# Kernel optimization log

Hardware: AMD Instinct MI355X
Metric: run time of the kernel (lower is better)

The kernel has to match this reference:

```python
import jax, jax.numpy as jnp
import numpy as np

NUM_HEADS = 16


def setup_inputs() -> dict:
    key = jax.random.key(0)
    ks = jax.random.split(key, 7)
    E = 1024
    s = 0.02
    return {
        "x": jax.random.normal(ks[0], (2, 2048, E), dtype=jnp.float32),
        "Wq": jax.random.normal(ks[1], (E, E), dtype=jnp.float32) * s,
        "bq": jax.random.normal(ks[2], (E,), dtype=jnp.float32) * s,
        "Wk": jax.random.normal(ks[3], (E, E), dtype=jnp.float32) * s,
        "bk": jax.random.normal(ks[4], (E,), dtype=jnp.float32) * s,
        "Wv": jax.random.normal(ks[5], (E, E), dtype=jnp.float32) * s,
        "bv": jax.random.normal(ks[6], (E,), dtype=jnp.float32) * s,
    }


def reference(x, Wq, bq, Wk, bk, Wv, bv):
    b, s, e = x.shape
    h = NUM_HEADS
    d = e // h  # head_dim = 64
    # nn.Linear: y = x @ W^T + b
    q = x @ Wq.T + bq
    k = x @ Wk.T + bk
    v = x @ Wv.T + bv
    # Faithful reshape chain from the source: (b,s,e)->(b,s,h,d)->(-1,s,d)
    # (raw reshape, NO transpose, matching the original buggy layout)
    q = q.reshape(b, s, h, d).reshape(-1, s, d)
    k = k.reshape(b, s, h, d).reshape(-1, s, d)
    v = v.reshape(b, s, h, d).reshape(-1, s, d)
    # Scaled scores; note the source returns qk @ v (softmax result discarded)
    scale = 1.0 / np.sqrt(d).astype(np.float32)
    qk = jnp.einsum('bqd,bkd->bqk', q, k) * scale  # [b*h, s, s]
    out = jnp.einsum('bqk,bkd->bqd', qk, v)        # [b*h, s, d]
    return out
```

## Files before the change

### kernel.cpp

```cpp
#include <hip/hip_runtime.h>
#include <hip/hip_bf16.h>


#define E_DIM 1024
#define N_ROWS 4096

typedef __attribute__((ext_vector_type(8))) short bf16x8;
typedef __attribute__((ext_vector_type(4))) float f32x4;

#define QB_U 0
#define XB_U 12582912
#define WB_U 16777216
#define P_F  9961472

__device__ __forceinline__ unsigned short f2b(float f) {
    union { float f; unsigned int i; } c; c.f = f;
    unsigned int r = c.i + 0x7FFFu + ((c.i >> 16) & 1u);
    return (unsigned short)(r >> 16);
}

__device__ __forceinline__ uint4 pack8(const f32x4 a, const f32x4 b) {
    uint4 o;
    o.x = (unsigned)f2b(a[0]) | ((unsigned)f2b(a[1]) << 16);
    o.y = (unsigned)f2b(a[2]) | ((unsigned)f2b(a[3]) << 16);
    o.z = (unsigned)f2b(b[0]) | ((unsigned)f2b(b[1]) << 16);
    o.w = (unsigned)f2b(b[2]) | ((unsigned)f2b(b[3]) << 16);
    return o;
}

__device__ __forceinline__ uint2 packfrag(const f32x4 a, float b) {
    uint2 v;
    v.x = (unsigned)f2b(a[0] + b) | ((unsigned)f2b(a[1] + b) << 16);
    v.y = (unsigned)f2b(a[2] + b) | ((unsigned)f2b(a[3] + b) << 16);
    return v;
}

typedef __attribute__((address_space(1))) const void* gptr_t;
typedef __attribute__((address_space(3))) void* lptr_t;
__device__ __forceinline__ void gl_lds16(const void* g, void* l) {
    __builtin_amdgcn_global_load_lds((gptr_t)g, (lptr_t)l, 16, 0, 0);
}

__device__ __forceinline__ int sw_idx(int row, int r) {
    return row * 64 + (((((r) >> 3) & 7) ^ (row & 7)) << 3) + (r & 7);
}

__device__ __forceinline__ int sw128(int row, int r) {
    return row * 128 + ((((r >> 3) ^ (row & 7)) & 15) << 3) + (r & 7);
}

__global__ __launch_bounds__(256) void cvt_bf16(
    const float* __restrict__ x,  const float* __restrict__ wq,
    const float* __restrict__ wk, const float* __restrict__ wv,
    unsigned short* __restrict__ dst0)
{
    const int seg = blockIdx.y;
    const float* __restrict__ src;
    unsigned short* __restrict__ dst;
    if (seg < 4) { src = x + (size_t)seg * 1048576; dst = dst0 + (size_t)seg * 1048576; }
    else {
        src = (seg == 4) ? wq : (seg == 5) ? wk : wv;
        dst = dst0 + 4194304 + (size_t)(seg - 4) * 1048576;
    }
    const int i = blockIdx.x * 256 + threadIdx.x;
    const float4 a = *(const float4*)(src + (size_t)i * 8);
    const float4 b = *(const float4*)(src + (size_t)i * 8 + 4);
    uint4 o;
    o.x = (unsigned)f2b(a.x) | ((unsigned)f2b(a.y) << 16);
    o.y = (unsigned)f2b(a.z) | ((unsigned)f2b(a.w) << 16);
    o.z = (unsigned)f2b(b.x) | ((unsigned)f2b(b.y) << 16);
    o.w = (unsigned)f2b(b.z) | ((unsigned)f2b(b.w) << 16);
    *(uint4*)(dst + (size_t)i * 8) = o;
}

__device__ __forceinline__ void gemm_loop(
    const unsigned short* __restrict__ Xb, const unsigned short* __restrict__ W,
    unsigned short* Als, unsigned short* Bls,
    int m0, int n0, int w, int lane, f32x4 (&acc)[4][4])
{
    const int quad = lane >> 4;
    const int fm   = lane & 15;
    const int sw8  = fm & 7;
    const int srow = lane >> 3;
    const int skc  = ((lane & 7) ^ (lane >> 3)) * 8;
    const int wm = (w >> 1) * 64;
    const int wn = (w & 1) * 64;

    for (int k0 = 0; k0 < E_DIM; k0 += 64) {
        #pragma unroll
        for (int c = 0; c < 4; ++c) {
            const int r = w * 32 + c * 8;
            gl_lds16((const void*)(Xb + (size_t)(m0 + r + srow) * E_DIM + k0 + skc),
                     (void*)((char*)Als + r * 128 + lane * 16));
            gl_lds16((const void*)(W + (size_t)(n0 + r + srow) * E_DIM + k0 + skc),
                     (void*)((char*)Bls + r * 128 + lane * 16));
        }
        __syncthreads();

        #pragma unroll
        for (int kk = 0; kk < 2; ++kk) {
            const int slot = ((kk * 4 + quad) ^ sw8) * 8;
            bf16x8 af[4], bf[4];
            #pragma unroll
            for (int t = 0; t < 4; ++t) {
                af[t] = *(const bf16x8*)(Als + (wm + t * 16 + fm) * 64 + slot);
                bf[t] = *(const bf16x8*)(Bls + (wn + t * 16 + fm) * 64 + slot);
            }
            #pragma unroll
            for (int rt = 0; rt < 4; ++rt)
                #pragma unroll
                for (int ct = 0; ct < 4; ++ct)
                    acc[rt][ct] = __builtin_amdgcn_mfma_f32_16x16x32_bf16(
                        af[rt], bf[ct], acc[rt][ct], 0, 0, 0);
        }
        __syncthreads();
    }
}

__global__ __launch_bounds__(256, 3) void qkvkt768(
    const unsigned short* __restrict__ Xb,
    const unsigned short* __restrict__ Wb,
    const float* __restrict__ bq, const float* __restrict__ bk,
    const float* __restrict__ bv,
    unsigned short* __restrict__ qkv,
    float* __restrict__ P)
{
    __shared__ __align__(16) unsigned short S[16384];

    const int b    = blockIdx.x;
    const int tid  = threadIdx.x;
    const int w    = tid >> 6;
    const int lane = tid & 63;
    const int quad = lane >> 4;
    const int fm   = lane & 15;
    const int sw8  = fm & 7;
    const int rbase = quad * 4;
    const int srow = lane >> 3;
    const int skc  = ((lane & 7) ^ (lane >> 3)) * 8;

    if (b >= 512) {
        const int idx = b - 512;
        const int m0 = (idx & 31) * 128;
        const int n0 = (idx >> 5) * 128;
        const int wm = (w >> 1) * 64;
        const int wn = (w & 1) * 64;

        f32x4 acc[4][4];
        #pragma unroll
        for (int i = 0; i < 4; ++i)
            #pragma unroll
            for (int j = 0; j < 4; ++j)
                acc[i][j] = f32x4{0.f, 0.f, 0.f, 0.f};

        gemm_loop(Xb, Wb, S, S + 8192, m0, n0, w, lane, acc);

        float bcol[4];
        #pragma unroll
        for (int ct = 0; ct < 4; ++ct) bcol[ct] = bq[n0 + wn + ct * 16 + fm];

        #pragma unroll
        for (int rt = 0; rt < 4; ++rt) {
            #pragma unroll
            for (int ct = 0; ct < 4; ++ct) {
                #pragma unroll
                for (int r = 0; r < 4; ++r) {
                    const int row = m0 + wm + rt * 16 + rbase + r;
                    const int col = n0 + wn + ct * 16 + fm;
                    qkv[(size_t)row * E_DIM + col] = f2b(acc[rt][ct][r] + bcol[ct]);
                }
            }
        }
        return;
    }

    const int bx = b >> 4;
    const int hy = b & 15;
    const int m0 = bx * 128;
    const int n0 = hy * 64;
    const unsigned short* __restrict__ WK = Wb + 1048576;
    const unsigned short* __restrict__ WV = Wb + 2097152;

    unsigned short* Xls = S;
    unsigned short* Kls = S + 8192;
    unsigned short* Vls = S + 12288;

    const int wm = w * 32;

    f32x4 acck[2][4], accv[2][4];
    #pragma unroll
    for (int t = 0; t < 2; ++t)
        #pragma unroll
        for (int n = 0; n < 4; ++n) {
            acck[t][n] = f32x4{0.f, 0.f, 0.f, 0.f};
            accv[t][n] = f32x4{0.f, 0.f, 0.f, 0.f};
        }

    for (int k0 = 0; k0 < E_DIM; k0 += 64) {
        #pragma unroll
        for (int c = 0; c < 4; ++c) {
            const int r = w * 32 + c * 8;
            gl_lds16((const void*)(Xb + (size_t)(m0 + r + srow) * E_DIM + k0 + skc),
                     (void*)((char*)Xls + r * 128 + lane * 16));
        }
        #pragma unroll
        for (int c = 0; c < 2; ++c) {
            const int r = w * 16 + c * 8;
            gl_lds16((const void*)(WK + (size_t)(n0 + r + srow) * E_DIM + k0 + skc),
                     (void*)((char*)Kls + r * 128 + lane * 16));
            gl_lds16((const void*)(WV + (size_t)(n0 + r + srow) * E_DIM + k0 + skc),
                     (void*)((char*)Vls + r * 128 + lane * 16));
        }
        __syncthreads();

        #pragma unroll
        for (int kk = 0; kk < 2; ++kk) {
            const int slot = ((kk * 4 + quad) ^ sw8) * 8;
            bf16x8 af[2], bk_[4], bv_[4];
            #pragma unroll
            for (int t = 0; t < 2; ++t)
                af[t] = *(const bf16x8*)(Xls + (wm + t * 16 + fm) * 64 + slot);
            #pragma unroll
            for (int n = 0; n < 4; ++n) {
                bk_[n] = *(const bf16x8*)(Kls + (n * 16 + fm) * 64 + slot);
                bv_[n] = *(const bf16x8*)(Vls + (n * 16 + fm) * 64 + slot);
            }
            #pragma unroll
            for (int t = 0; t < 2; ++t)
                #pragma unroll
                for (int n = 0; n < 4; ++n) {
                    acck[t][n] = __builtin_amdgcn_mfma_f32_16x16x32_bf16(
                        af[t], bk_[n], acck[t][n], 0, 0, 0);
                    accv[t][n] = __builtin_amdgcn_mfma_f32_16x16x32_bf16(
                        af[t], bv_[n], accv[t][n], 0, 0, 0);
                }
        }
        __syncthreads();
    }

    float bcK[4], bcV[4];
    #pragma unroll
    for (int n = 0; n < 4; ++n) {
        bcK[n] = bk[n0 + n * 16 + fm];
        bcV[n] = bv[n0 + n * 16 + fm];
    }

    unsigned short* Kt = S;
    unsigned short* Vt = S + 8192;

    #pragma unroll
    for (int t = 0; t < 2; ++t)
        #pragma unroll
        for (int n = 0; n < 4; ++n) {
            const int e  = n * 16 + fm;
            const int r0 = wm + t * 16 + rbase;
            *(uint2*)(Kt + sw128(e, r0)) = packfrag(acck[t][n], bcK[n]);
            *(uint2*)(Vt + sw128(e, r0)) = packfrag(accv[t][n], bcV[n]);
        }
    __syncthreads();

    f32x4 tacc[4];
    #pragma unroll
    for (int n = 0; n < 4; ++n) tacc[n] = f32x4{0.f, 0.f, 0.f, 0.f};
    #pragma unroll
    for (int kk = 0; kk < 4; ++kk) {
        const int slot = (((kk * 4 + quad) ^ sw8) & 15) << 3;
        const bf16x8 af = *(const bf16x8*)(Vt + (w * 16 + fm) * 128 + slot);
        #pragma unroll
        for (int n = 0; n < 4; ++n) {
            const bf16x8 bf = *(const bf16x8*)(Kt + (n * 16 + fm) * 128 + slot);
            tacc[n] = __builtin_amdgcn_mfma_f32_16x16x32_bf16(af, bf, tacc[n], 0, 0, 0);
        }
    }

    float* __restrict__ Pout = P + ((size_t)bx * 16 + hy) * 4096;
    #pragma unroll
    for (int n = 0; n < 4; ++n)
        #pragma unroll
        for (int r = 0; r < 4; ++r)
            Pout[(size_t)(w * 16 + rbase + r) * 64 + n * 16 + fm] = tacc[n][r];
}

__global__ __launch_bounds__(256, 2) void qT_fused(
    const unsigned short* __restrict__ qkv,
    const float* __restrict__ P,
    float* __restrict__ out)
{
    __shared__ __align__(16) unsigned short Als[128 * 64];
    __shared__ __align__(16) unsigned short Tls[64 * 64];

    const int b    = blockIdx.x;
    const int i    = (b & 7) + ((b >> 3) & 3) * 8;
    const int sub  = b >> 5;
    const int r0   = (i * 16 + sub) * 128;
    const int tid  = threadIdx.x;
    const int w    = tid >> 6;
    const int lane = tid & 63;
    const int quad = lane >> 4;
    const int fm   = lane & 15;
    const int sw8  = fm & 7;

    const unsigned short* __restrict__ Qb = qkv + QB_U + (size_t)r0 * 64;

    const int soff = (lane >> 3) * 64 + (((lane & 7) ^ (lane >> 3)) << 3);
    #pragma unroll
    for (int c = 0; c < 4; ++c)
        gl_lds16((const void*)(Qb + (w * 4 + c) * 512 + soff),
                 (void*)((char*)Als + (w * 4 + c) * 1024));

    {
        const int d  = tid >> 2;
        const int e0 = (tid & 3) << 4;
        const float* p = P + (size_t)i * 65536 + (size_t)d * 64 + e0;
        f32x4 s0{0.f,0.f,0.f,0.f}, s1{0.f,0.f,0.f,0.f};
        f32x4 s2{0.f,0.f,0.f,0.f}, s3{0.f,0.f,0.f,0.f};
        #pragma unroll
        for (int c = 0; c < 16; ++c) {
            s0 += *(const f32x4*)(p + (size_t)c * 4096);
            s1 += *(const f32x4*)(p + (size_t)c * 4096 + 4);
            s2 += *(const f32x4*)(p + (size_t)c * 4096 + 8);
            s3 += *(const f32x4*)(p + (size_t)c * 4096 + 12);
        }
        const int c0 = e0 >> 3;
        *(uint4*)(Tls + d * 64 + ((c0 ^ (d & 7)) << 3))       = pack8(s0, s1);
        *(uint4*)(Tls + d * 64 + (((c0 + 1) ^ (d & 7)) << 3)) = pack8(s2, s3);
    }
    __syncthreads();

    bf16x8 af[2][2], bf[4][2];
    #pragma unroll
    for (int mt = 0; mt < 2; ++mt)
        #pragma unroll
        for (int kk = 0; kk < 2; ++kk)
            af[mt][kk] = *(const bf16x8*)(Als + (w * 32 + mt * 16 + fm) * 64
                                          + (((kk * 4 + quad) ^ sw8) << 3));
    #pragma unroll
    for (int nt = 0; nt < 4; ++nt)
        #pragma unroll
        for (int kk = 0; kk < 2; ++kk)
            bf[nt][kk] = *(const bf16x8*)(Tls + (nt * 16 + fm) * 64
                                          + (((kk * 4 + quad) ^ sw8) << 3));

    f32x4 acc[2][4];
    #pragma unroll
    for (int mt = 0; mt < 2; ++mt)
        #pragma unroll
        for (int nt = 0; nt < 4; ++nt)
            acc[mt][nt] = f32x4{0.f, 0.f, 0.f, 0.f};

    #pragma unroll
    for (int kk = 0; kk < 2; ++kk)
        #pragma unroll
        for (int mt = 0; mt < 2; ++mt)
            #pragma unroll
            for (int nt = 0; nt < 4; ++nt)
                acc[mt][nt] = __builtin_amdgcn_mfma_f32_16x16x32_bf16(
                    af[mt][kk], bf[nt][kk], acc[mt][nt], 0, 0, 0);

    const int rbase = (lane >> 4) * 4;
    #pragma unroll
    for (int mt = 0; mt < 2; ++mt) {
        #pragma unroll
        for (int nt = 0; nt < 4; ++nt) {
            #pragma unroll
            for (int r = 0; r < 4; ++r) {
                const int row = r0 + w * 32 + mt * 16 + rbase + r;
                const int col = nt * 16 + fm;
                out[(size_t)row * 64 + col] = 0.125f * acc[mt][nt][r];
            }
        }
    }
}

extern "C" void kernel_launch(void* const* d_in, const int* in_sizes, int n_in,
                              void* d_out, int out_size, void* d_ws, size_t ws_size,
                              hipStream_t stream)
{
    const float* x  = (const float*)d_in[0];
    const float* Wq = (const float*)d_in[1];
    const float* bq = (const float*)d_in[2];
    const float* Wk = (const float*)d_in[3];
    const float* bk = (const float*)d_in[4];
    const float* Wv = (const float*)d_in[5];
    const float* bv = (const float*)d_in[6];
    float* wsf = (float*)d_ws;
    unsigned short* wsu = (unsigned short*)d_ws;
    float* out = (float*)d_out;

    dim3 gCvt(512, 7);
    cvt_bf16<<<gCvt, 256, 0, stream>>>(x, Wq, Wk, Wv, wsu + XB_U);

    qkvkt768<<<768, 256, 0, stream>>>(wsu + XB_U, wsu + WB_U,
                                      bq, bk, bv, wsu, wsf + P_F);

    qT_fused<<<512, 256, 0, stream>>>(wsu, wsf + P_F, out);
}
```

Baseline: 124.9 us.

## Reduce K^T V partials once via last-block atomic counter in projection kernel

Moves the 16-way reduction of the partial K^T·V products out of qT_fused, where each of the 16 sub-blocks for a head group redid the same sum, into the projection kernel. There the last block to finish each group, found through an agent-scope atomic counter, sums the partials once and writes a bf16 tile. qT_fused then loads that precomputed tile straight into LDS with async global-to-LDS copies. This cuts redundant fp32 reads from the final kernel at the cost of an atomic, extra fences and a serialized tail reduction in the producer. Counters are zeroed in the conversion kernel.

```diff
diff --git a/kernel.cpp b/kernel.cpp
--- a/kernel.cpp
+++ b/kernel.cpp
@@ -11,7 +11,9 @@
 #define QB_U 0
 #define XB_U 12582912
 #define WB_U 16777216
+#define TB_U 24117504
 #define P_F  9961472
+#define BAR_F 12058624
 
 __device__ __forceinline__ unsigned short f2b(float f) {
     union { float f; unsigned int i; } c; c.f = f;
@@ -52,8 +54,10 @@
 __global__ __launch_bounds__(256) void cvt_bf16(
     const float* __restrict__ x,  const float* __restrict__ wq,
     const float* __restrict__ wk, const float* __restrict__ wv,
-    unsigned short* __restrict__ dst0)
+    unsigned short* __restrict__ dst0, unsigned* __restrict__ cnt)
 {
+    if (blockIdx.x == 0 && blockIdx.y == 0 && threadIdx.x < 32)
+        cnt[threadIdx.x] = 0u;
     const int seg = blockIdx.y;
     const float* __restrict__ src;
     unsigned short* __restrict__ dst;
@@ -123,7 +127,9 @@
     const float* __restrict__ bq, const float* __restrict__ bk,
     const float* __restrict__ bv,
     unsigned short* __restrict__ qkv,
-    float* __restrict__ P)
+    float* __restrict__ P,
+    unsigned short* __restrict__ TB,
+    unsigned* __restrict__ cnt)
 {
     __shared__ __align__(16) unsigned short S[16384];
 
@@ -278,15 +284,42 @@
         #pragma unroll
         for (int r = 0; r < 4; ++r)
             Pout[(size_t)(w * 16 + rbase + r) * 64 + n * 16 + fm] = tacc[n][r];
+
+    __syncthreads();
+    if (tid == 0) {
+        __threadfence();
+        const unsigned old = __hip_atomic_fetch_add(
+            &cnt[bx], 1u, __ATOMIC_ACQ_REL, __HIP_MEMORY_SCOPE_AGENT);
+        ((int*)S)[0] = (old == 15u) ? 1 : 0;
+    }
+    __syncthreads();
+    if (((int*)S)[0]) {
+        __threadfence();
+        const int d  = tid >> 2;
+        const int e0 = (tid & 3) << 4;
+        const float* p = P + (size_t)bx * 65536 + (size_t)d * 64 + e0;
+        f32x4 s0{0.f,0.f,0.f,0.f}, s1{0.f,0.f,0.f,0.f};
+        f32x4 s2{0.f,0.f,0.f,0.f}, s3{0.f,0.f,0.f,0.f};
+        #pragma unroll
+        for (int c = 0; c < 16; ++c) {
+            s0 += *(const f32x4*)(p + (size_t)c * 4096);
+            s1 += *(const f32x4*)(p + (size_t)c * 4096 + 4);
+            s2 += *(const f32x4*)(p + (size_t)c * 4096 + 8);
+            s3 += *(const f32x4*)(p + (size_t)c * 4096 + 12);
+        }
+        unsigned short* tb = TB + (size_t)bx * 4096 + d * 64 + e0;
+        *(uint4*)(tb)     = pack8(s0, s1);
+        *(uint4*)(tb + 8) = pack8(s2, s3);
+    }
 }
 
 __global__ __launch_bounds__(256, 2) void qT_fused(
     const unsigned short* __restrict__ qkv,
-    const float* __restrict__ P,
+    const unsigned short* __restrict__ TB,
     float* __restrict__ out)
 {
     __shared__ __align__(16) unsigned short Als[128 * 64];
-    __shared__ __align__(16) unsigned short Tls[64 * 64];
+    __shared__ __align__(16) unsigned short Bls[64 * 64];
 
     const int b    = blockIdx.x;
     const int i    = (b & 7) + ((b >> 3) & 3) * 8;
@@ -300,30 +333,17 @@
     const int sw8  = fm & 7;
 
     const unsigned short* __restrict__ Qb = qkv + QB_U + (size_t)r0 * 64;
+    const unsigned short* __restrict__ Tb = TB + (size_t)i * 4096;
 
     const int soff = (lane >> 3) * 64 + (((lane & 7) ^ (lane >> 3)) << 3);
     #pragma unroll
     for (int c = 0; c < 4; ++c)
         gl_lds16((const void*)(Qb + (w * 4 + c) * 512 + soff),
                  (void*)((char*)Als + (w * 4 + c) * 1024));
-
-    {
-        const int d  = tid >> 2;
-        const int e0 = (tid & 3) << 4;
-        const float* p = P + (size_t)i * 65536 + (size_t)d * 64 + e0;
-        f32x4 s0{0.f,0.f,0.f,0.f}, s1{0.f,0.f,0.f,0.f};
-        f32x4 s2{0.f,0.f,0.f,0.f}, s3{0.f,0.f,0.f,0.f};
-        #pragma unroll
-        for (int c = 0; c < 16; ++c) {
-            s0 += *(const f32x4*)(p + (size_t)c * 4096);
-            s1 += *(const f32x4*)(p + (size_t)c * 4096 + 4);
-            s2 += *(const f32x4*)(p + (size_t)c * 4096 + 8);
-            s3 += *(const f32x4*)(p + (size_t)c * 4096 + 12);
-        }
-        const int c0 = e0 >> 3;
-        *(uint4*)(Tls + d * 64 + ((c0 ^ (d & 7)) << 3))       = pack8(s0, s1);
-        *(uint4*)(Tls + d * 64 + (((c0 + 1) ^ (d & 7)) << 3)) = pack8(s2, s3);
-    }
+    #pragma unroll
+    for (int c = 0; c < 2; ++c)
+        gl_lds16((const void*)(Tb + (w * 2 + c) * 512 + soff),
+                 (void*)((char*)Bls + (w * 2 + c) * 1024));
     __syncthreads();
 
     bf16x8 af[2][2], bf[4][2];
@@ -337,7 +357,7 @@
     for (int nt = 0; nt < 4; ++nt)
         #pragma unroll
         for (int kk = 0; kk < 2; ++kk)
-            bf[nt][kk] = *(const bf16x8*)(Tls + (nt * 16 + fm) * 64
+            bf[nt][kk] = *(const bf16x8*)(Bls + (nt * 16 + fm) * 64
                                           + (((kk * 4 + quad) ^ sw8) << 3));
 
     f32x4 acc[2][4];
@@ -385,12 +405,14 @@
     float* wsf = (float*)d_ws;
     unsigned short* wsu = (unsigned short*)d_ws;
     float* out = (float*)d_out;
+    unsigned* cnt = (unsigned*)(wsf + BAR_F);
 
     dim3 gCvt(512, 7);
-    cvt_bf16<<<gCvt, 256, 0, stream>>>(x, Wq, Wk, Wv, wsu + XB_U);
+    cvt_bf16<<<gCvt, 256, 0, stream>>>(x, Wq, Wk, Wv, wsu + XB_U, cnt);
 
     qkvkt768<<<768, 256, 0, stream>>>(wsu + XB_U, wsu + WB_U,
-                                      bq, bk, bv, wsu, wsf + P_F);
-
-    qT_fused<<<512, 256, 0, stream>>>(wsu, wsf + P_F, out);
-}
+                                      bq, bk, bv, wsu, wsf + P_F,
+                                      wsu + TB_U, cnt);
+
+    qT_fused<<<512, 256, 0, stream>>>(wsu, wsu + TB_U, out);
+}
```

Measured after the change: 176.4 us. 1.41x slower.
